# Kernel optimization log

Measured on AMD Instinct MI355X. Metric: run time of the kernel, lower is better.

The kernel has to match this reference:

```python
import jax, jax.numpy as jnp
import numpy as np

B, S, D = 4, 2048, 1024
H, DK, DV = 16, 64, 64
LN_EPS = 1e-5


def setup_inputs() -> dict:
    key = jax.random.key(0)
    ks = jax.random.split(key, 16)
    s = 0.02
    inp = {
        "Q": jax.random.normal(ks[0], (B, S, D), jnp.float32),
        "K": jax.random.normal(ks[1], (B, S, D), jnp.float32),
        "V": jax.random.normal(ks[2], (B, S, D), jnp.float32),
        "mask": jnp.tril(jnp.ones((S, S), jnp.int32)),  # causal 2D mask
        "W_Q": jax.random.normal(ks[3], (D, H * DK), jnp.float32) * s,
        "b_Q": jnp.zeros((H * DK,), jnp.float32),
        "W_K": jax.random.normal(ks[4], (D, H * DK), jnp.float32) * s,
        "b_K": jnp.zeros((H * DK,), jnp.float32),
        "W_V": jax.random.normal(ks[5], (D, H * DV), jnp.float32) * s,
        "b_V": jnp.zeros((H * DV,), jnp.float32),
        "W_O": jax.random.normal(ks[6], (H * DV, D), jnp.float32) * s,
        "b_O": jnp.zeros((D,), jnp.float32),
        "ln_gamma": jnp.ones((D,), jnp.float32),
        "ln_beta": jnp.zeros((D,), jnp.float32),
    }
    return inp


def reference(Q, K, V, mask, W_Q, b_Q, W_K, b_K, W_V, b_V, W_O, b_O, ln_gamma, ln_beta):
    residual = Q
    # projections -> [B, H, S, d]
    q = (Q @ W_Q + b_Q).reshape(B, S, H, DK).transpose(0, 2, 1, 3)
    k = (K @ W_K + b_K).reshape(B, S, H, DK).transpose(0, 2, 1, 3)
    v = (V @ W_V + b_V).reshape(B, S, H, DV).transpose(0, 2, 1, 3)
    # scaled dot-product attention with explicit [B,H,S,S] scores
    scores = jnp.einsum("bhqd,bhkd->bhqk", q, k) / jnp.sqrt(jnp.float32(DK))
    m = mask[None, None, :, :]  # 2D mask -> [1,1,S,S] as in torch code
    scores = jnp.where(m == 0, jnp.float32(-1e9), scores)
    attn = jax.nn.softmax(scores, axis=-1)
    out = jnp.einsum("bhqk,bhkd->bhqd", attn, v)
    out = out.transpose(0, 2, 1, 3).reshape(B, S, H * DV)
    out = out @ W_O + b_O
    # layer norm over residual + out
    x = residual + out
    mu = jnp.mean(x, axis=-1, keepdims=True)
    var = jnp.mean(jnp.square(x - mu), axis=-1, keepdims=True)
    y = (x - mu) / jnp.sqrt(var + LN_EPS) * ln_gamma + ln_beta
    return y, attn
```

## Files before the change

### kernel.cpp

```cpp
#include <hip/hip_runtime.h>
#include <hip/hip_bf16.h>
#include <math.h>

#define NB 4
#define NS 2048
#define ND 1024
#define NH 16

typedef __attribute__((ext_vector_type(8))) __bf16 bf16x8;
typedef __attribute__((ext_vector_type(4))) float f32x4;
typedef __attribute__((ext_vector_type(8))) unsigned short ushort8_t;

#define VMCNT0() asm volatile("s_waitcnt vmcnt(0)" ::: "memory")
#define VMCNT2() asm volatile("s_waitcnt vmcnt(2)" ::: "memory")
#define VMCNT4() asm volatile("s_waitcnt vmcnt(4)" ::: "memory")
#define LGKM0()  asm volatile("s_waitcnt lgkmcnt(0)" ::: "memory")
#define BAR()    __builtin_amdgcn_s_barrier()

__device__ __forceinline__ unsigned short f2bf(float f){
  union { float f; unsigned int u; } v; v.f = f;
  unsigned int r = (v.u + 0x7FFFu + ((v.u >> 16) & 1u)) >> 16;
  return (unsigned short)r;
}
__device__ __forceinline__ float bf2f(unsigned short u){
  union { unsigned int i; float f; } v; v.i = ((unsigned int)u) << 16;
  return v.f;
}
__device__ __forceinline__ f32x4 mfma16(bf16x8 a, bf16x8 b, f32x4 c){
  return __builtin_amdgcn_mfma_f32_16x16x32_bf16(a, b, c, 0, 0, 0);
}
__device__ __forceinline__ bf16x8 lds_frag(const unsigned short* p){
  ushort8_t u = *reinterpret_cast<const ushort8_t*>(p);
  return __builtin_bit_cast(bf16x8, u);
}
__device__ __forceinline__ void gl16(const unsigned short* g, unsigned short* l){
  __builtin_amdgcn_global_load_lds(
      (const __attribute__((address_space(1))) void*)g,
      (__attribute__((address_space(3))) void*)l, 16, 0, 0);
}

__global__ __launch_bounds__(256)
void k_convert3(const float* __restrict__ a, const float* __restrict__ b,
                const float* __restrict__ c, unsigned short* __restrict__ oa,
                unsigned short* __restrict__ ob, unsigned short* __restrict__ oc,
                int n4){
  int i = blockIdx.x * 256 + threadIdx.x;
  if (i >= n4) return;
  const float* in = (blockIdx.y == 0) ? a : (blockIdx.y == 1) ? b : c;
  unsigned short* out = (blockIdx.y == 0) ? oa : (blockIdx.y == 1) ? ob : oc;
  float4 v = reinterpret_cast<const float4*>(in)[i];
  ushort4 o;
  o.x = f2bf(v.x); o.y = f2bf(v.y); o.z = f2bf(v.z); o.w = f2bf(v.w);
  reinterpret_cast<ushort4*>(out)[i] = o;
}

__global__ __launch_bounds__(256)
void k_transpose4(const float* __restrict__ w0, const float* __restrict__ w1,
                  const float* __restrict__ w2, const float* __restrict__ w3,
                  unsigned short* __restrict__ out){
  __shared__ float t[32][33];
  const float* in = (blockIdx.z == 0) ? w0 : (blockIdx.z == 1) ? w1 :
                    (blockIdx.z == 2) ? w2 : w3;
  unsigned short* o = out + (size_t)blockIdx.z * 1048576;
  const int k0 = blockIdx.x * 32, n0 = blockIdx.y * 32;
  const int tx = threadIdx.x & 31, ty = threadIdx.x >> 5;
  for (int r = ty; r < 32; r += 8)
    t[r][tx] = in[(size_t)(k0 + r) * 1024 + n0 + tx];
  __syncthreads();
  for (int r = ty; r < 32; r += 8)
    o[(size_t)(n0 + r) * 1024 + k0 + tx] = f2bf(t[tx][r]);
}

__global__ __launch_bounds__(256)
void k_gemm_qkv(const unsigned short* __restrict__ A0,
                const unsigned short* __restrict__ A1,
                const unsigned short* __restrict__ A2,
                const unsigned short* __restrict__ WT,
                const float* __restrict__ b0, const float* __restrict__ b1,
                const float* __restrict__ b2,
                unsigned short* __restrict__ o0,
                unsigned short* __restrict__ o1,
                unsigned short* __restrict__ o2)
{
  constexpr int K = 1024;
  __shared__ unsigned short a_s[128 * 64];
  __shared__ unsigned short b_s[128 * 64];
  const int bm = blockIdx.x;
  const int gid = blockIdx.y >> 3, bn = blockIdx.y & 7;
  const unsigned short* A = (gid == 0) ? A0 : (gid == 1) ? A1 : A2;
  const unsigned short* BT = WT + (size_t)gid * 1048576;
  const float* bias = (gid == 0) ? b0 : (gid == 1) ? b1 : b2;
  unsigned short* outp = (gid == 0) ? o0 : (gid == 1) ? o1 : o2;

  const int tid = threadIdx.x, lane = tid & 63, w = tid >> 6;
  const int wr = w >> 1, wc = w & 1;
  const int l15 = lane & 15, l4 = lane >> 4;
  const int xsw = (l15 & 7) << 3;
  const int lr = lane >> 3;
  const int scol = ((lane & 7) << 3) ^ (lr << 3);

  const f32x4 z4 = {0.f, 0.f, 0.f, 0.f};
  f32x4 acc[4][4];
  #pragma unroll
  for (int i = 0; i < 4; ++i)
    #pragma unroll
    for (int j = 0; j < 4; ++j) acc[i][j] = z4;

  const size_t abase = (size_t)(bm * 128) * K;
  const size_t bbase = (size_t)(bn * 128) * K;

  for (int kt = 0; kt < 16; ++kt){
    __syncthreads();
    #pragma unroll
    for (int i = 0; i < 4; ++i){
      const int row = w * 32 + i * 8 + lr;
      gl16(&A[abase + (size_t)row * K + kt * 64 + scol], &a_s[(w * 32 + i * 8) * 64]);
      gl16(&BT[bbase + (size_t)row * K + kt * 64 + scol], &b_s[(w * 32 + i * 8) * 64]);
    }
    __syncthreads();
    #pragma unroll
    for (int ks = 0; ks < 2; ++ks){
      const int cb = (ks * 32 + l4 * 8) ^ xsw;
      bf16x8 af[4], bfr[4];
      #pragma unroll
      for (int mf = 0; mf < 4; ++mf)
        af[mf] = lds_frag(&a_s[(wr * 64 + mf * 16 + l15) * 64 + cb]);
      #pragma unroll
      for (int nf = 0; nf < 4; ++nf)
        bfr[nf] = lds_frag(&b_s[(wc * 64 + nf * 16 + l15) * 64 + cb]);
      #pragma unroll
      for (int mf = 0; mf < 4; ++mf)
        #pragma unroll
        for (int nf = 0; nf < 4; ++nf)
          acc[mf][nf] = mfma16(af[mf], bfr[nf], acc[mf][nf]);
    }
  }

  #pragma unroll
  for (int mf = 0; mf < 4; ++mf){
    #pragma unroll
    for (int nf = 0; nf < 4; ++nf){
      const int n = bn * 128 + wc * 64 + nf * 16 + l15;
      const float bv = bias[n];
      #pragma unroll
      for (int r = 0; r < 4; ++r){
        const int m = bm * 128 + wr * 64 + mf * 16 + l4 * 4 + r;
        const float v = acc[mf][nf][r] + bv;
        const int b = m >> 11, s = m & 2047, h = n >> 6, d = n & 63;
        if (gid <= 1)
          outp[((((size_t)b * NH + h) * NS + s) << 6) + d] = f2bf(v);
        else
          outp[(((size_t)b * NH + h) * 64 + d) * NS + s] = f2bf(v);
      }
    }
  }
}

__global__ __launch_bounds__(256)
void k_gemm_o(const unsigned short* __restrict__ A,
              const unsigned short* __restrict__ BT,
              const float* __restrict__ bias,
              const float* __restrict__ resid,
              unsigned short* __restrict__ outp)
{
  constexpr int K = 1024;
  __shared__ unsigned short a_s[128 * 64];
  __shared__ unsigned short b_s[128 * 64];
  const int bm = blockIdx.x, bn = blockIdx.y;
  const int tid = threadIdx.x, lane = tid & 63, w = tid >> 6;
  const int wr = w >> 1, wc = w & 1;
  const int l15 = lane & 15, l4 = lane >> 4;
  const int xsw = (l15 & 7) << 3;
  const int lr = lane >> 3;
  const int scol = ((lane & 7) << 3) ^ (lr << 3);

  const f32x4 z4 = {0.f, 0.f, 0.f, 0.f};
  f32x4 acc[4][4];
  #pragma unroll
  for (int i = 0; i < 4; ++i)
    #pragma unroll
    for (int j = 0; j < 4; ++j) acc[i][j] = z4;

  const size_t abase = (size_t)(bm * 128) * K;
  const size_t bbase = (size_t)(bn * 128) * K;

  for (int kt = 0; kt < 16; ++kt){
    __syncthreads();
    #pragma unroll
    for (int i = 0; i < 4; ++i){
      const int row = w * 32 + i * 8 + lr;
      gl16(&A[abase + (size_t)row * K + kt * 64 + scol], &a_s[(w * 32 + i * 8) * 64]);
      gl16(&BT[bbase + (size_t)row * K + kt * 64 + scol], &b_s[(w * 32 + i * 8) * 64]);
    }
    __syncthreads();
    #pragma unroll
    for (int ks = 0; ks < 2; ++ks){
      const int cb = (ks * 32 + l4 * 8) ^ xsw;
      bf16x8 af[4], bfr[4];
      #pragma unroll
      for (int mf = 0; mf < 4; ++mf)
        af[mf] = lds_frag(&a_s[(wr * 64 + mf * 16 + l15) * 64 + cb]);
      #pragma unroll
      for (int nf = 0; nf < 4; ++nf)
        bfr[nf] = lds_frag(&b_s[(wc * 64 + nf * 16 + l15) * 64 + cb]);
      #pragma unroll
      for (int mf = 0; mf < 4; ++mf)
        #pragma unroll
        for (int nf = 0; nf < 4; ++nf)
          acc[mf][nf] = mfma16(af[mf], bfr[nf], acc[mf][nf]);
    }
  }

  #pragma unroll
  for (int mf = 0; mf < 4; ++mf){
    #pragma unroll
    for (int nf = 0; nf < 4; ++nf){
      const int n = bn * 128 + wc * 64 + nf * 16 + l15;
      const float bv = bias[n];
      #pragma unroll
      for (int r = 0; r < 4; ++r){
        const int m = bm * 128 + wr * 64 + mf * 16 + l4 * 4 + r;
        const size_t idx = (size_t)m * ND + n;
        outp[idx] = f2bf(acc[mf][nf][r] + bv + resid[idx]);
      }
    }
  }
}

__global__ __launch_bounds__(256, 4)
void k_attn(const unsigned short* __restrict__ qh,
            const unsigned short* __restrict__ kh,
            const unsigned short* __restrict__ vt,
            unsigned short* __restrict__ ctx,
            float* __restrict__ attn)
{
  __shared__ unsigned short k_s0[64 * 64];
  __shared__ unsigned short k_s1[64 * 64];
  __shared__ unsigned short kv2[64 * 64];
  __shared__ unsigned short p_s[64][72];

  const int id = blockIdx.x + 32 * blockIdx.y;
  const int swz = (id & 7) * 256 + (id >> 3);
  const int bh = swz >> 5;
  const int qb = 31 - (swz & 31);
  const int q0 = qb * 64;
  const int tid = threadIdx.x, lane = tid & 63, w = tid >> 6;
  const int l15 = lane & 15, l4 = lane >> 4;
  const int xsw = (l15 & 7) << 3;
  const int lr = lane >> 3;
  const int scol = ((lane & 7) << 3) ^ (lr << 3);
  const f32x4 z4 = {0.f, 0.f, 0.f, 0.f};
  const size_t kvb = (size_t)bh * NS * 64;

  bf16x8 qf[2];
  {
    const unsigned short* qp = &qh[kvb + (size_t)(q0 + w * 16 + l15) * 64];
    qf[0] = lds_frag(qp + l4 * 8);
    qf[1] = lds_frag(qp + 32 + l4 * 8);
  }

  const float SC = 0.125f * 1.44269504088896341f;
  const int ncomp = qb + 1;
  const int growb = q0 + w * 16 + l4 * 4;

  float lp[4] = {0.f, 0.f, 0.f, 0.f};

  #pragma unroll
  for (int i = 0; i < 2; ++i)
    gl16(&kh[kvb + (size_t)(w * 16 + i * 8 + lr) * 64 + scol],
         &k_s0[(w * 16 + i * 8) * 64]);
  if (ncomp > 1){
    #pragma unroll
    for (int i = 0; i < 2; ++i)
      gl16(&kh[kvb + (size_t)(64 + w * 16 + i * 8 + lr) * 64 + scol],
           &k_s1[(w * 16 + i * 8) * 64]);
    VMCNT2();
  } else {
    VMCNT0();
  }
  BAR();

  int cbi = 0;
  for (int kt = 0; kt < ncomp; ++kt){
    const bool haveNext = (kt + 1 < ncomp);
    const bool havePre  = (kt + 2 < ncomp);
    if (havePre){
      int nbi = cbi + 2; if (nbi >= 3) nbi -= 3;
      unsigned short* nb = (nbi == 0) ? k_s0 : ((nbi == 1) ? k_s1 : kv2);
      #pragma unroll
      for (int i = 0; i < 2; ++i)
        gl16(&kh[kvb + (size_t)((kt + 2) * 64 + w * 16 + i * 8 + lr) * 64 + scol],
             &nb[(w * 16 + i * 8) * 64]);
    }
    const unsigned short* cb_ = (cbi == 0) ? k_s0 : ((cbi == 1) ? k_s1 : kv2);
    f32x4 sc4[4];
    #pragma unroll
    for (int cf = 0; cf < 4; ++cf) sc4[cf] = z4;
    __builtin_amdgcn_s_setprio(1);
    #pragma unroll
    for (int ks = 0; ks < 2; ++ks){
      const int cb = (ks * 32 + l4 * 8) ^ xsw;
      #pragma unroll
      for (int cf = 0; cf < 4; ++cf){
        const bf16x8 bk = lds_frag(&cb_[(cf * 16 + l15) * 64 + cb]);
        sc4[cf] = mfma16(qf[ks], bk, sc4[cf]);
      }
    }
    __builtin_amdgcn_s_setprio(0);
    if (kt == ncomp - 1){
      #pragma unroll
      for (int cf = 0; cf < 4; ++cf){
        const int gcol = kt * 64 + cf * 16 + l15;
        #pragma unroll
        for (int r = 0; r < 4; ++r)
          lp[r] += (gcol <= growb + r) ? exp2f(sc4[cf][r] * SC) : 0.f;
      }
    } else {
      #pragma unroll
      for (int cf = 0; cf < 4; ++cf)
        #pragma unroll
        for (int r = 0; r < 4; ++r)
          lp[r] += exp2f(sc4[cf][r] * SC);
    }
    if (havePre){ VMCNT2(); } else if (haveNext){ VMCNT0(); }
    LGKM0();
    BAR();
    cbi = (cbi == 2) ? 0 : cbi + 1;
  }

  float rl[4];
  #pragma unroll
  for (int r = 0; r < 4; ++r){
    float t = lp[r];
    t += __shfl_xor(t, 1);
    t += __shfl_xor(t, 2);
    t += __shfl_xor(t, 4);
    t += __shfl_xor(t, 8);
    rl[r] = 1.f / t;
  }

  f32x4 oacc[4];
  #pragma unroll
  for (int nf = 0; nf < 4; ++nf) oacc[nf] = z4;
  float* arow = attn + (size_t)bh * NS * NS;

  #pragma unroll
  for (int i = 0; i < 2; ++i)
    gl16(&kh[kvb + (size_t)(w * 16 + i * 8 + lr) * 64 + scol],
         &k_s0[(w * 16 + i * 8) * 64]);
  VMCNT0();
  BAR();
  int cur = 0;

  for (int kt = 0; kt < ncomp; ++kt){
    const bool haveK = (kt + 1 < ncomp);
    unsigned short* kcur = cur ? k_s1 : k_s0;
    unsigned short* knxt = cur ? k_s0 : k_s1;
    #pragma unroll
    for (int i = 0; i < 2; ++i){
      const int row = w * 16 + i * 8 + lr;
      gl16(&vt[kvb + (size_t)row * NS + kt * 64 + scol], &kv2[(w * 16 + i * 8) * 64]);
    }
    if (haveK){
      #pragma unroll
      for (int i = 0; i < 2; ++i)
        gl16(&kh[kvb + (size_t)((kt + 1) * 64 + w * 16 + i * 8 + lr) * 64 + scol],
             &knxt[(w * 16 + i * 8) * 64]);
    }
    f32x4 sc4[4];
    #pragma unroll
    for (int cf = 0; cf < 4; ++cf) sc4[cf] = z4;
    __builtin_amdgcn_s_setprio(1);
    #pragma unroll
    for (int ks = 0; ks < 2; ++ks){
      const int cb = (ks * 32 + l4 * 8) ^ xsw;
      #pragma unroll
      for (int cf = 0; cf < 4; ++cf){
        const bf16x8 bk = lds_frag(&kcur[(cf * 16 + l15) * 64 + cb]);
        sc4[cf] = mfma16(qf[ks], bk, sc4[cf]);
      }
    }
    __builtin_amdgcn_s_setprio(0);
    if (kt == ncomp - 1){
      #pragma unroll
      for (int cf = 0; cf < 4; ++cf){
        const int gcol = kt * 64 + cf * 16 + l15;
        #pragma unroll
        for (int r = 0; r < 4; ++r){
          const float a = (gcol <= growb + r) ? exp2f(sc4[cf][r] * SC) * rl[r] : 0.f;
          p_s[w * 16 + l4 * 4 + r][cf * 16 + l15] = f2bf(a);
        }
      }
    } else {
      #pragma unroll
      for (int cf = 0; cf < 4; ++cf)
        #pragma unroll
        for (int r = 0; r < 4; ++r)
          p_s[w * 16 + l4 * 4 + r][cf * 16 + l15] = f2bf(exp2f(sc4[cf][r] * SC) * rl[r]);
    }
    if (haveK){ VMCNT2(); } else { VMCNT0(); }
    LGKM0();
    BAR();
    #pragma unroll
    for (int it = 0; it < 4; ++it){
      const int row = it * 16 + (tid >> 4);
      const int c0 = (tid & 15) * 4;
      const ushort4 u = *reinterpret_cast<const ushort4*>(&p_s[row][c0]);
      f32x4 f4;
      f4[0] = bf2f(u.x); f4[1] = bf2f(u.y); f4[2] = bf2f(u.z); f4[3] = bf2f(u.w);
      __builtin_nontemporal_store(
          f4, reinterpret_cast<f32x4*>(&arow[(size_t)(q0 + row) * NS + kt * 64 + c0]));
    }
    __builtin_amdgcn_s_setprio(1);
    #pragma unroll
    for (int ks2 = 0; ks2 < 2; ++ks2){
      const bf16x8 ap = lds_frag(&p_s[w * 16 + l15][ks2 * 32 + l4 * 8]);
      const int cb = (ks2 * 32 + l4 * 8) ^ xsw;
      #pragma unroll
      for (int nf = 0; nf < 4; ++nf){
        const bf16x8 bv = lds_frag(&kv2[(nf * 16 + l15) * 64 + cb]);
        oacc[nf] = mfma16(ap, bv, oacc[nf]);
      }
    }
    __builtin_amdgcn_s_setprio(0);
    if (haveK){
      VMCNT4();
      BAR();
    }
    cur ^= 1;
  }

  const int b = bh >> 4, h = bh & 15;
  #pragma unroll
  for (int nf = 0; nf < 4; ++nf){
    #pragma unroll
    for (int r = 0; r < 4; ++r){
      const int s = growb + r;
      ctx[((size_t)b * NS + s) * ND + h * 64 + nf * 16 + l15] = f2bf(oacc[nf][r]);
    }
  }

  const int zc0 = ncomp * 64;
  if (zc0 < NS){
    const f32x4 zz = {0.f, 0.f, 0.f, 0.f};
    for (int r = 0; r < 64; ++r){
      float* rp = arow + (size_t)(q0 + r) * NS;
      for (int c = zc0 + tid * 4; c < NS; c += 1024)
        __builtin_nontemporal_store(zz, reinterpret_cast<f32x4*>(rp + c));
    }
  }
}

__global__ __launch_bounds__(256)
void k_ln(const unsigned short* __restrict__ x, const float* __restrict__ gamma,
          const float* __restrict__ beta, float* __restrict__ y){
  const int row = blockIdx.x;
  const ushort4 u = reinterpret_cast<const ushort4*>(x + (size_t)row * ND)[threadIdx.x];
  float v0 = bf2f(u.x), v1 = bf2f(u.y), v2 = bf2f(u.z), v3 = bf2f(u.w);
  float s = v0 + v1 + v2 + v3;
  float ss = v0 * v0 + v1 * v1 + v2 * v2 + v3 * v3;
  #pragma unroll
  for (int off = 32; off; off >>= 1){
    s += __shfl_xor(s, off);
    ss += __shfl_xor(ss, off);
  }
  __shared__ float rs[4], rss[4];
  const int w = threadIdx.x >> 6;
  if ((threadIdx.x & 63) == 0){ rs[w] = s; rss[w] = ss; }
  __syncthreads();
  s = rs[0] + rs[1] + rs[2] + rs[3];
  ss = rss[0] + rss[1] + rss[2] + rss[3];
  const float mu = s * (1.f / ND);
  const float var = ss * (1.f / ND) - mu * mu;
  const float rstd = rsqrtf(var + 1e-5f);
  const float4 g = reinterpret_cast<const float4*>(gamma)[threadIdx.x];
  const float4 be = reinterpret_cast<const float4*>(beta)[threadIdx.x];
  float4 o;
  o.x = (v0 - mu) * rstd * g.x + be.x;
  o.y = (v1 - mu) * rstd * g.y + be.y;
  o.z = (v2 - mu) * rstd * g.z + be.z;
  o.w = (v3 - mu) * rstd * g.w + be.w;
  reinterpret_cast<float4*>(y + (size_t)row * ND)[threadIdx.x] = o;
}

extern "C" void kernel_launch(void* const* d_in, const int* in_sizes, int n_in,
                              void* d_out, int out_size, void* d_ws, size_t ws_size,
                              hipStream_t stream){
  const float* Q   = (const float*)d_in[0];
  const float* Kin = (const float*)d_in[1];
  const float* V   = (const float*)d_in[2];
  const float* W_Q = (const float*)d_in[4];
  const float* b_Q = (const float*)d_in[5];
  const float* W_K = (const float*)d_in[6];
  const float* b_K = (const float*)d_in[7];
  const float* W_V = (const float*)d_in[8];
  const float* b_V = (const float*)d_in[9];
  const float* W_O = (const float*)d_in[10];
  const float* b_O = (const float*)d_in[11];
  const float* g   = (const float*)d_in[12];
  const float* be  = (const float*)d_in[13];

  char* ws = (char*)d_ws;
  const size_t SZ = (size_t)8192 * 1024 * 2;
  unsigned short* Qb = (unsigned short*)(ws);
  unsigned short* Kb = (unsigned short*)(ws + SZ);
  unsigned short* Vb = (unsigned short*)(ws + 2 * SZ);
  unsigned short* WT = (unsigned short*)(ws + 3 * SZ);
  unsigned short* qh = (unsigned short*)(ws + 3 * SZ + 4 * 2097152);
  unsigned short* kh = qh + (size_t)8388608;
  unsigned short* vt = kh + (size_t)8388608;
  unsigned short* ctx = Qb;
  unsigned short* x = Kb;
  float* y = (float*)d_out;
  float* attn = y + (size_t)NB * NS * ND;

  const int n4 = (NB * NS * ND) / 4;
  k_convert3<<<dim3(n4 / 256, 3), 256, 0, stream>>>(Q, Kin, V, Qb, Kb, Vb, n4);
  k_transpose4<<<dim3(32, 32, 4), 256, 0, stream>>>(W_Q, W_K, W_V, W_O, WT);

  k_gemm_qkv<<<dim3(64, 24), 256, 0, stream>>>(Qb, Kb, Vb, WT, b_Q, b_K, b_V,
                                               qh, kh, vt);

  k_attn<<<dim3(32, 64), 256, 0, stream>>>(qh, kh, vt, ctx, attn);

  k_gemm_o<<<dim3(64, 8), 256, 0, stream>>>(ctx, WT + 3 * 1048576, b_O, Q, x);

  k_ln<<<NB * NS, 256, 0, stream>>>(x, g, be, y);
}
```

Baseline: 389.6 us.

## Swizzle P tile in LDS, raise attention occupancy, add nontemporal loads and stores

The attention kernel's P staging buffer drops its 72-column padding for a dense 64x64 layout with an XOR swizzle on the column index. This cuts LDS use per block and removes bank conflicts without padding. The launch bound goes from 4 to 5 blocks per CU, which could force register spills. Separately, the convert kernel reads K and V with nontemporal loads (Q keeps a normal load, likely because Q is read again as the residual), and the layernorm writes its output with nontemporal stores.

Result: slower. 400.2 us (+2.7%).

```diff
diff --git a/kernel.cpp b/kernel.cpp
--- a/kernel.cpp
+++ b/kernel.cpp
@@ -46,9 +46,15 @@
                 int n4){
   int i = blockIdx.x * 256 + threadIdx.x;
   if (i >= n4) return;
-  const float* in = (blockIdx.y == 0) ? a : (blockIdx.y == 1) ? b : c;
+  float4 v;
+  if (blockIdx.y == 0){
+    v = reinterpret_cast<const float4*>(a)[i];
+  } else {
+    const float* in = (blockIdx.y == 1) ? b : c;
+    f32x4 t = __builtin_nontemporal_load(reinterpret_cast<const f32x4*>(in) + i);
+    v.x = t[0]; v.y = t[1]; v.z = t[2]; v.w = t[3];
+  }
   unsigned short* out = (blockIdx.y == 0) ? oa : (blockIdx.y == 1) ? ob : oc;
-  float4 v = reinterpret_cast<const float4*>(in)[i];
   ushort4 o;
   o.x = f2bf(v.x); o.y = f2bf(v.y); o.z = f2bf(v.z); o.w = f2bf(v.w);
   reinterpret_cast<ushort4*>(out)[i] = o;
@@ -227,7 +233,7 @@
   }
 }
 
-__global__ __launch_bounds__(256, 4)
+__global__ __launch_bounds__(256, 5)
 void k_attn(const unsigned short* __restrict__ qh,
             const unsigned short* __restrict__ kh,
             const unsigned short* __restrict__ vt,
@@ -237,7 +243,7 @@
   __shared__ unsigned short k_s0[64 * 64];
   __shared__ unsigned short k_s1[64 * 64];
   __shared__ unsigned short kv2[64 * 64];
-  __shared__ unsigned short p_s[64][72];
+  __shared__ unsigned short p_s[64 * 64];
 
   const int id = blockIdx.x + 32 * blockIdx.y;
   const int swz = (id & 7) * 256 + (id >> 3);
@@ -388,15 +394,19 @@
         #pragma unroll
         for (int r = 0; r < 4; ++r){
           const float a = (gcol <= growb + r) ? exp2f(sc4[cf][r] * SC) * rl[r] : 0.f;
-          p_s[w * 16 + l4 * 4 + r][cf * 16 + l15] = f2bf(a);
+          const int row = w * 16 + l4 * 4 + r;
+          p_s[row * 64 + ((cf * 16 + l15) ^ ((row & 7) << 3))] = f2bf(a);
         }
       }
     } else {
       #pragma unroll
       for (int cf = 0; cf < 4; ++cf)
         #pragma unroll
-        for (int r = 0; r < 4; ++r)
-          p_s[w * 16 + l4 * 4 + r][cf * 16 + l15] = f2bf(exp2f(sc4[cf][r] * SC) * rl[r]);
+        for (int r = 0; r < 4; ++r){
+          const float a = exp2f(sc4[cf][r] * SC) * rl[r];
+          const int row = w * 16 + l4 * 4 + r;
+          p_s[row * 64 + ((cf * 16 + l15) ^ ((row & 7) << 3))] = f2bf(a);
+        }
     }
     if (haveK){ VMCNT2(); } else { VMCNT0(); }
     LGKM0();
@@ -405,7 +415,8 @@
     for (int it = 0; it < 4; ++it){
       const int row = it * 16 + (tid >> 4);
       const int c0 = (tid & 15) * 4;
-      const ushort4 u = *reinterpret_cast<const ushort4*>(&p_s[row][c0]);
+      const ushort4 u = *reinterpret_cast<const ushort4*>(
+          &p_s[row * 64 + (c0 ^ ((row & 7) << 3))]);
       f32x4 f4;
       f4[0] = bf2f(u.x); f4[1] = bf2f(u.y); f4[2] = bf2f(u.z); f4[3] = bf2f(u.w);
       __builtin_nontemporal_store(
@@ -414,7 +425,9 @@
     __builtin_amdgcn_s_setprio(1);
     #pragma unroll
     for (int ks2 = 0; ks2 < 2; ++ks2){
-      const bf16x8 ap = lds_frag(&p_s[w * 16 + l15][ks2 * 32 + l4 * 8]);
+      const int prow = w * 16 + l15;
+      const bf16x8 ap = lds_frag(
+          &p_s[prow * 64 + ((ks2 * 32 + l4 * 8) ^ ((prow & 7) << 3))]);
       const int cb = (ks2 * 32 + l4 * 8) ^ xsw;
       #pragma unroll
       for (int nf = 0; nf < 4; ++nf){
@@ -475,12 +488,13 @@
   const float rstd = rsqrtf(var + 1e-5f);
   const float4 g = reinterpret_cast<const float4*>(gamma)[threadIdx.x];
   const float4 be = reinterpret_cast<const float4*>(beta)[threadIdx.x];
-  float4 o;
-  o.x = (v0 - mu) * rstd * g.x + be.x;
-  o.y = (v1 - mu) * rstd * g.y + be.y;
-  o.z = (v2 - mu) * rstd * g.z + be.z;
-  o.w = (v3 - mu) * rstd * g.w + be.w;
-  reinterpret_cast<float4*>(y + (size_t)row * ND)[threadIdx.x] = o;
+  f32x4 o;
+  o[0] = (v0 - mu) * rstd * g.x + be.x;
+  o[1] = (v1 - mu) * rstd * g.y + be.y;
+  o[2] = (v2 - mu) * rstd * g.z + be.z;
+  o[3] = (v3 - mu) * rstd * g.w + be.w;
+  __builtin_nontemporal_store(
+      o, reinterpret_cast<f32x4*>(y + (size_t)row * ND) + threadIdx.x);
 }
 
 extern "C" void kernel_launch(void* const* d_in, const int* in_sizes, int n_in,
```
